# Performance work log

Measured on AMD Instinct MI355X. Metric: run time of the kernel, lower is better.

## Reference

```python
import jax, jax.numpy as jnp
import numpy as np
from jax import lax
from functools import lru_cache

WS = 8       # window size
SS = 4       # shift size
NH = 8       # attention heads
D_STATE = 64
D_CONV = 4
CHUNK = 256  # SSD chunk length


def _ln(x, w, b, eps=1e-5):
    mu = x.mean(-1, keepdims=True)
    xc = x - mu
    var = (xc * xc).mean(-1, keepdims=True)
    return xc * lax.rsqrt(var + eps) * w + b


@lru_cache(maxsize=None)
def _rel_index(ws):
    coords = np.stack(np.meshgrid(np.arange(ws), np.arange(ws), indexing='ij')).reshape(2, -1)
    rel = (coords[:, :, None] - coords[:, None, :]).transpose(1, 2, 0)
    rel[:, :, 0] += ws - 1
    rel[:, :, 1] += ws - 1
    rel[:, :, 0] *= 2 * ws - 1
    return jnp.asarray(rel.sum(-1))  # (N, N)


@lru_cache(maxsize=None)
def _shift_mask(H, W, ws, ss):
    img = np.zeros((H, W))
    cnt = 0
    for hs in (slice(0, -ws), slice(-ws, -ss), slice(-ss, None)):
        for wsl in (slice(0, -ws), slice(-ws, -ss), slice(-ss, None)):
            img[hs, wsl] = cnt
            cnt += 1
    mw = img.reshape(H // ws, ws, W // ws, ws).transpose(0, 2, 1, 3).reshape(-1, ws * ws)
    diff = mw[:, None, :] - mw[:, :, None]
    return jnp.asarray(np.where(diff != 0, -100.0, 0.0).astype(np.float32))  # (nW,N,N)


def _segsum(a):
    # a: (...,Q) -> (...,Q,Q) with S[i,j] = sum_{k=j+1..i} a_k for i>=j else -inf
    T = a.shape[-1]
    cs = jnp.cumsum(a, -1)
    d = cs[..., :, None] - cs[..., None, :]
    return jnp.where(jnp.tril(jnp.ones((T, T), bool)), d, -jnp.inf)


def _ssd(xd, a, Bc, Cc):
    # Chunked SSD scan (Mamba2). xd=(B,L,H,P) pre-multiplied by dt; a=dt*A (B,L,H);
    # Bc,Cc=(B,L,N) with ngroups=1 (shared across heads).
    B_, L, H_, P = xd.shape
    Q = CHUNK
    c = L // Q
    N = Bc.shape[-1]
    xd = xd.reshape(B_, c, Q, H_, P)
    a = a.reshape(B_, c, Q, H_).transpose(0, 3, 1, 2)  # (B,H,c,Q)
    Bc = Bc.reshape(B_, c, Q, N)
    Cc = Cc.reshape(B_, c, Q, N)
    A_cs = jnp.cumsum(a, -1)
    Lm = jnp.exp(_segsum(a))  # (B,H,c,Q,Q) causal decay mask
    Yd = jnp.einsum('bcln,bcsn,bhcls,bcshp->bclhp', Cc, Bc, Lm, xd)
    dec_st = jnp.exp(A_cs[..., -1:] - A_cs)
    states = jnp.einsum('bcsn,bhcs,bcshp->bchpn', Bc, dec_st, xd)  # (B,c,H,P,N)
    chunk_dec = jnp.exp(A_cs[..., -1])  # (B,H,c)

    def step(h, inp):
        dec, st = inp
        return h * dec[..., None, None] + st, h

    h0 = jnp.zeros((B_, H_, P, N), xd.dtype)
    _, st_in = lax.scan(step, h0, (chunk_dec.transpose(2, 0, 1), states.transpose(1, 0, 2, 3, 4)))
    st_in = st_in.transpose(1, 0, 2, 3, 4)  # (B,c,H,P,N) state entering each chunk
    Yo = jnp.einsum('bcln,bchpn,bhcl->bclhp', Cc, st_in, jnp.exp(A_cs))
    return (Yd + Yo).reshape(B_, L, H_, P)


def _mamba2(x, win, conv_w, conv_b, dt_bias, a_log, d_skip, norm_w, wout):
    Bb, L, _ = x.shape
    conv_dim = conv_w.shape[0]
    d_inner = conv_dim - 2 * D_STATE
    nh = a_log.shape[0]
    hd = d_inner // nh
    zxbcdt = x @ win
    z = zxbcdt[..., :d_inner]
    xBC = zxbcdt[..., d_inner:d_inner + conv_dim]
    dt = zxbcdt[..., -nh:]
    # causal depthwise conv (kernel D_CONV) + SiLU
    xp = jnp.pad(xBC, ((0, 0), (D_CONV - 1, 0), (0, 0)))
    xc = conv_b + sum(xp[:, k:k + L, :] * conv_w[:, k] for k in range(D_CONV))
    xc = jax.nn.silu(xc)
    xs = xc[..., :d_inner].reshape(Bb, L, nh, hd)
    Bm = xc[..., d_inner:d_inner + D_STATE]
    Cm = xc[..., d_inner + D_STATE:]
    dt = jax.nn.softplus(dt + dt_bias)  # (B,L,nh)
    a = dt * (-jnp.exp(a_log))
    y = _ssd(xs * dt[..., None], a, Bm, Cm)
    y = y + d_skip[None, None, :, None] * xs
    y = y.reshape(Bb, L, d_inner)
    u = y * jax.nn.silu(z)  # gated RMSNorm
    u = u * lax.rsqrt((u * u).mean(-1, keepdims=True) + 1e-5) * norm_w
    return u @ wout


def reference(x, ln1_w, ln1_b, ns_w, ns_b, m_win, m_conv_w, m_conv_b, m_dt_bias,
              m_a_log, m_d, m_norm_w, m_wout, tm_w1, tm_b1, tm_w2, tm_b2, nt_w, nt_b,
              qkv_w, qkv_b, rpb, gate_w, gate_b, proj_w, proj_b,
              cg_w1a, cg_b1a, cg_w2a, cg_b2a, cg_w1m, cg_b1m, cg_w2m, cg_b2m, cg_wf, cg_bf,
              ln2_w, ln2_b, mlp_w1, mlp_b1, mlp_w2, mlp_b2, H, W):
    twoB, L, C = x.shape
    B = twoB // 2
    shortcut = x
    xn = _ln(x, ln1_w, ln1_b)
    # ---- Branch A: factorized SSM (spatial Mamba2 + symmetric temporal MLP fusion) ----
    xns = _ln(xn, ns_w, ns_b)
    sp = _mamba2(xns, m_win, m_conv_w, m_conv_b, m_dt_bias, m_a_log, m_d, m_norm_w, m_wout) + xn
    f0, f1 = sp[:B], sp[B:]

    def tmix(a, b):
        h = jax.nn.silu(jnp.concatenate([a, b], -1) @ tm_w1 + tm_b1)
        return h @ tm_w2 + tm_b2

    f0 = _ln(f0 + tmix(f0, f1), nt_w, nt_b)
    f1 = _ln(f1 + tmix(f1, f0), nt_w, nt_b)
    xm = jnp.concatenate([f0, f1], 0)
    # ---- Branch B: shifted-window gated attention ----
    N = WS * WS
    x2 = jnp.roll(xn.reshape(twoB, H, W, C), (-SS, -SS), (1, 2))
    xw = x2.reshape(twoB, H // WS, WS, W // WS, WS, C).transpose(0, 1, 3, 2, 4, 5).reshape(-1, N, C)
    qkv = (xw @ qkv_w + qkv_b).reshape(-1, N, 3, NH, C // NH).transpose(2, 0, 3, 1, 4)
    q, k, v = qkv[0], qkv[1], qkv[2]  # (nWB, NH, N, hd)
    attn = (q * (C // NH) ** -0.5) @ k.transpose(0, 1, 3, 2)
    attn = attn + rpb[_rel_index(WS)].transpose(2, 0, 1)[None]
    mask = _shift_mask(H, W, WS, SS)
    nW = mask.shape[0]
    attn = (attn.reshape(twoB, nW, NH, N, N) + mask[None, :, None]).reshape(-1, NH, N, N)
    attn = jax.nn.softmax(attn, -1)
    out = (attn @ v).transpose(0, 2, 1, 3).reshape(-1, N, C)
    out = out * jax.nn.sigmoid(xw @ gate_w + gate_b)  # per-token gate
    out = out @ proj_w + proj_b
    out = out.reshape(twoB, H // WS, W // WS, WS, WS, C).transpose(0, 1, 3, 2, 4, 5).reshape(twoB, H, W, C)
    xa = jnp.roll(out, (SS, SS), (1, 2)).reshape(twoB, L, C)
    # ---- Cross-gating fusion (1x1-conv bottleneck gates == per-position MLPs) ----
    gm = jax.nn.sigmoid(jax.nn.relu(xa @ cg_w1a + cg_b1a) @ cg_w2a + cg_b2a)
    ga = jax.nn.sigmoid(jax.nn.relu(xm @ cg_w1m + cg_b1m) @ cg_w2m + cg_b2m)
    fused = jnp.concatenate([xm * gm, xa * ga], -1) @ cg_wf + cg_bf
    xo = shortcut + fused
    # ---- MLP ----
    h = jax.nn.gelu(_ln(xo, ln2_w, ln2_b) @ mlp_w1 + mlp_b1, approximate=False)
    return xo + h @ mlp_w2 + mlp_b2


def setup_inputs():
    key = jax.random.key(0)
    ks = iter(jax.random.split(key, 64))

    def nrm(shape, s=0.02):
        return jax.random.normal(next(ks), shape, jnp.float32) * s

    C, d_inner, nh_m = 256, 512, 8
    twoB, H, W = 8, 64, 64
    L = H * W
    conv_dim = d_inner + 2 * D_STATE
    inp = dict(
        x=jax.random.normal(next(ks), (twoB, L, C), jnp.float32),
        ln1_w=jnp.ones(C), ln1_b=jnp.zeros(C),
        ns_w=jnp.ones(C), ns_b=jnp.zeros(C),
        m_win=nrm((C, 2 * d_inner + 2 * D_STATE + nh_m)),
        m_conv_w=nrm((conv_dim, D_CONV), 0.1), m_conv_b=jnp.zeros(conv_dim),
        m_dt_bias=nrm((nh_m,), 0.1),
        m_a_log=jnp.log(jnp.arange(1, nh_m + 1, dtype=jnp.float32)),
        m_d=jnp.ones(nh_m), m_norm_w=jnp.ones(d_inner), m_wout=nrm((d_inner, C)),
        tm_w1=nrm((2 * C, C)), tm_b1=jnp.zeros(C), tm_w2=nrm((C, C)), tm_b2=jnp.zeros(C),
        nt_w=jnp.ones(C), nt_b=jnp.zeros(C),
        qkv_w=nrm((C, 3 * C)), qkv_b=jnp.zeros(3 * C),
        rpb=nrm(((2 * WS - 1) ** 2, NH)),
        gate_w=nrm((C, C)), gate_b=jnp.zeros(C),
        proj_w=nrm((C, C)), proj_b=jnp.zeros(C),
        cg_w1a=nrm((C, C // 4)), cg_b1a=jnp.zeros(C // 4), cg_w2a=nrm((C // 4, C)), cg_b2a=jnp.zeros(C),
        cg_w1m=nrm((C, C // 4)), cg_b1m=jnp.zeros(C // 4), cg_w2m=nrm((C // 4, C)), cg_b2m=jnp.zeros(C),
        cg_wf=nrm((2 * C, C)), cg_bf=jnp.zeros(C),
        ln2_w=jnp.ones(C), ln2_b=jnp.zeros(C),
        mlp_w1=nrm((C, 4 * C)), mlp_b1=jnp.zeros(4 * C),
        mlp_w2=nrm((4 * C, C)), mlp_b2=jnp.zeros(C),
        H=H, W=W,
    )
    return inp
```

## Files before the change

kernel.cpp:

```cpp
#include <hip/hip_runtime.h>
#include <math.h>


#define DEVI static __device__ __forceinline__
typedef unsigned short u16;
typedef unsigned int   u32;
typedef __attribute__((ext_vector_type(8))) short s16x8;
typedef __attribute__((ext_vector_type(4))) float f32x4;

DEVI float sigm_(float x){ return 1.f/(1.f+__expf(-x)); }
DEVI float silu_(float x){ return x/(1.f+__expf(-x)); }
DEVI float wsum_(float v){
#pragma unroll
  for (int o=32;o>0;o>>=1) v += __shfl_xor(v,o,64);
  return v;
}

DEVI float b2f(u16 u){ union{u32 i; float f;} v; v.i = ((u32)u)<<16; return v.f; }
DEVI u16 f2b(float f){ union{float f; u32 i;} v; v.f=f; u32 r = v.i + 0x7fffu + ((v.i>>16)&1u); return (u16)(r>>16); }
DEVI float4 ld4(const float* p){ return *(const float4*)p; }
DEVI float4 ld4(const u16* p){
  uint2 r = *(const uint2*)p;
  return make_float4(b2f((u16)(r.x&0xffff)), b2f((u16)(r.x>>16)),
                     b2f((u16)(r.y&0xffff)), b2f((u16)(r.y>>16)));
}
DEVI void st4(u16* p, float a, float b, float c, float d){
  uint2 r; r.x = (u32)f2b(a) | ((u32)f2b(b)<<16); r.y = (u32)f2b(c) | ((u32)f2b(d)<<16);
  *(uint2*)p = r;
}
DEVI void ld8(const u16* p, float* f){
  uint4 r = *(const uint4*)p;
  f[0]=b2f((u16)(r.x&0xffff)); f[1]=b2f((u16)(r.x>>16));
  f[2]=b2f((u16)(r.y&0xffff)); f[3]=b2f((u16)(r.y>>16));
  f[4]=b2f((u16)(r.z&0xffff)); f[5]=b2f((u16)(r.z>>16));
  f[6]=b2f((u16)(r.w&0xffff)); f[7]=b2f((u16)(r.w>>16));
}
DEVI void st8(u16* p, const float* f){
  uint4 r;
  r.x=(u32)f2b(f[0])|((u32)f2b(f[1])<<16); r.y=(u32)f2b(f[2])|((u32)f2b(f[3])<<16);
  r.z=(u32)f2b(f[4])|((u32)f2b(f[5])<<16); r.w=(u32)f2b(f[6])|((u32)f2b(f[7])<<16);
  *(uint4*)p = r;
}
DEVI float tof(float v){ return v; }
DEVI float tof(u16 v){ return b2f(v); }
DEVI void sto(float* p, float v){ *p = v; }
DEVI void sto(u16* p, float v){ *p = f2b(v); }

DEVI int vswz(int row, int ch){ return ch ^ ((row&7) ^ ((row>>3)&7)); }

DEVI void gl16(const u16* g, u16* l){
  __builtin_amdgcn_global_load_lds(
      (const __attribute__((address_space(1))) u32*)g,
      (__attribute__((address_space(3))) u32*)l, 16, 0, 0);
}

DEVI int winmap_tok(int r){
  int win = r>>6, tk = r&63;
  int b = win>>6, wid = win&63;
  int h2 = ((wid>>3)<<3) + (tk>>3);
  int w2 = ((wid&7)<<3) + (tk&7);
  int hh = (h2+4)&63, wwp = (w2+4)&63;
  return b*4096 + hh*64 + wwp;
}

__global__ __launch_bounds__(256) void ln2x_k(
    const float* __restrict__ x, const float* __restrict__ w1, const float* __restrict__ b1,
    const float* __restrict__ w2, const float* __restrict__ b2,
    u16* __restrict__ xn, u16* __restrict__ xns)
{
  int tok = blockIdx.x*4 + (threadIdx.x>>6);
  int lane = threadIdx.x & 63;
  size_t base = (size_t)tok*256 + lane*4;
  float4 v = *(const float4*)(x + base);
  float mu = wsum_(v.x+v.y+v.z+v.w) * (1.f/256.f);
  float ax=v.x-mu, ay=v.y-mu, az=v.z-mu, aw=v.w-mu;
  float var = wsum_(ax*ax+ay*ay+az*az+aw*aw) * (1.f/256.f);
  float r = rsqrtf(var+1e-5f);
  float4 wv = *(const float4*)(w1+lane*4);
  float4 bv = *(const float4*)(b1+lane*4);
  float ox=ax*r*wv.x+bv.x, oy=ay*r*wv.y+bv.y, oz=az*r*wv.z+bv.z, ow=aw*r*wv.w+bv.w;
  st4(xn + base, ox, oy, oz, ow);
  float mu2 = wsum_(ox+oy+oz+ow)*(1.f/256.f);
  float bx=ox-mu2, by=oy-mu2, bz=oz-mu2, bw=ow-mu2;
  float var2 = wsum_(bx*bx+by*by+bz*bz+bw*bw)*(1.f/256.f);
  float r2 = rsqrtf(var2+1e-5f);
  float4 w2v = *(const float4*)(w2+lane*4);
  float4 b2v = *(const float4*)(b2+lane*4);
  st4(xns + base, bx*r2*w2v.x+b2v.x, by*r2*w2v.y+b2v.y, bz*r2*w2v.z+b2v.z, bw*r2*w2v.w+b2v.w);
}

template<typename IT>
__global__ __launch_bounds__(256) void ln_k(
    const IT* __restrict__ in, const float* __restrict__ w, const float* __restrict__ b,
    u16* __restrict__ outp)
{
  int tok = blockIdx.x*4 + (threadIdx.x>>6);
  int lane = threadIdx.x & 63;
  size_t base = (size_t)tok*256 + lane*4;
  float4 v = ld4(in + base);
  float mu = wsum_(v.x+v.y+v.z+v.w) * (1.f/256.f);
  float ax=v.x-mu, ay=v.y-mu, az=v.z-mu, aw=v.w-mu;
  float var = wsum_(ax*ax+ay*ay+az*az+aw*aw) * (1.f/256.f);
  float r = rsqrtf(var+1e-5f);
  float4 wv = *(const float4*)(w+lane*4);
  float4 bv = *(const float4*)(b+lane*4);
  st4(outp + base, ax*r*wv.x+bv.x, ay*r*wv.y+bv.y, az*r*wv.z+bv.z, aw*r*wv.w+bv.w);
}

struct WtD { const float* W; u16* Wt; int ldw, K, kb, nt; };
struct WtTab { WtD d[15]; };

__global__ __launch_bounds__(256) void wtall_k(WtTab tab)
{
  int loc = blockIdx.x;
  int r = 0;
#pragma unroll
  for (int i=0;i<15;i++){
    int cnt = tab.d[i].kb * tab.d[i].nt;
    if (loc >= cnt && r == i){ loc -= cnt; r = i+1; }
  }
  const float* W = tab.d[r].W;
  u16* Wt = tab.d[r].Wt;
  int ldw = tab.d[r].ldw, K = tab.d[r].K, kb = tab.d[r].kb;
  int k0 = (loc % kb)*32, n0 = (loc / kb)*32;
  __shared__ float tl[32][33];
  int t = threadIdx.x; int ty=t>>5, tx=t&31;
#pragma unroll
  for (int i=0;i<4;i++){
    int k = ty + i*8;
    tl[k][tx] = W[(size_t)(k0+k)*ldw + n0+tx];
  }
  __syncthreads();
#pragma unroll
  for (int i=0;i<4;i++){
    int n = ty + i*8;
    Wt[(size_t)(n0+n)*K + k0 + tx] = f2b(tl[tx][n]);
  }
}

enum { EPI_NONE=0, EPI_SILU=1, EPI_GELU=2, EPI_SIGMUL=3, EPI_ADD=4, EPI_RELU=5, EPI_SIGMOID=6 };

template<int BM, int BN, int EPI, bool WIN, bool WINST, typename OT, typename CT>
__global__ __launch_bounds__(256) void mgemm_k(
    const u16* __restrict__ A1, const u16* __restrict__ A2, int K1, int K2,
    const u16* __restrict__ Wt, const float* __restrict__ bias,
    const OT* other, CT* outp, int N, int r0)
{
  constexpr int MW = BM/32;
  constexpr int NWF = BN/32;
  constexpr int LA = BM/32;
  constexpr int LB = BN/32;
  __shared__ u16 As[BM][64];
  __shared__ u16 Bs[BN][64];
  int m0 = blockIdx.y*BM, n0 = blockIdx.x*BN;
  int t = threadIdx.x;
  int lane = t&63, w = t>>6;
  int wr = w>>1, wc = w&1;
  int K = K1 + K2;
  f32x4 acc[MW][NWF];
#pragma unroll
  for (int mi=0;mi<MW;mi++)
#pragma unroll
    for (int ni=0;ni<NWF;ni++) acc[mi][ni] = (f32x4){0.f,0.f,0.f,0.f};
  int srow = lane>>3;
  int cs   = ((lane&7) ^ srow)*8;
  size_t aoff1[LA], aoff2[LA];
#pragma unroll
  for (int i=0;i<LA;i++){
    int gr = m0 + i*32 + w*8 + srow;
    if (WIN) aoff1[i] = (size_t)winmap_tok(r0+gr)*K1;
    else { aoff1[i] = (size_t)gr*K1; aoff2[i] = (size_t)gr*K2; }
  }
  size_t boff[LB];
#pragma unroll
  for (int i=0;i<LB;i++)
    boff[i] = (size_t)(n0 + i*32 + w*8 + srow)*K;
  for (int k0=0; k0<K; k0+=64){
#pragma unroll
    for (int i=0;i<LA;i++){
      const u16* ap = (WIN || k0 < K1) ? A1 + aoff1[i] + k0 + cs
                                       : A2 + aoff2[i] + (k0-K1) + cs;
      gl16(ap, &As[i*32 + w*8][0]);
    }
#pragma unroll
    for (int i=0;i<LB;i++){
      gl16(Wt + boff[i] + k0 + cs, &Bs[i*32 + w*8][0]);
    }
    __syncthreads();
    int lg = lane>>4, li = lane&15;
#pragma unroll
    for (int kk=0;kk<2;kk++){
      s16x8 afr[MW], bfr[NWF];
#pragma unroll
      for (int mi=0;mi<MW;mi++){
        int lr = wr*(BM/2)+mi*16+li;
        afr[mi] = *(const s16x8*)&As[lr][(((kk<<2)+lg) ^ (lr&7))<<3];
      }
#pragma unroll
      for (int ni=0;ni<NWF;ni++){
        int lr = wc*(BN/2)+ni*16+li;
        bfr[ni] = *(const s16x8*)&Bs[lr][(((kk<<2)+lg) ^ (lr&7))<<3];
      }
#pragma unroll
      for (int mi=0;mi<MW;mi++)
#pragma unroll
        for (int ni=0;ni<NWF;ni++)
          acc[mi][ni] = __builtin_amdgcn_mfma_f32_16x16x32_bf16(afr[mi], bfr[ni], acc[mi][ni], 0,0,0);
    }
    __syncthreads();
  }
  int lg = lane>>4, li = lane&15;
#pragma unroll
  for (int mi=0;mi<MW;mi++){
#pragma unroll
    for (int ni=0;ni<NWF;ni++){
      int gn = n0 + wc*(BN/2) + ni*16 + li;
      float bv = bias ? bias[gn] : 0.f;
#pragma unroll
      for (int r=0;r<4;r++){
        int gm = m0 + wr*(BM/2) + mi*16 + lg*4 + r;
        float v = acc[mi][ni][r] + bv;
        size_t orow = WINST ? (size_t)winmap_tok(r0+gm) : (size_t)gm;
        size_t off = orow*N + gn;
        if (EPI==EPI_SILU)        v = silu_(v);
        else if (EPI==EPI_GELU)   v = 0.5f*v*(1.f+erff(v*0.70710678118654752f));
        else if (EPI==EPI_SIGMUL) v = tof(other[off])*sigm_(v);
        else if (EPI==EPI_ADD)    v = v + tof(other[off]);
        else if (EPI==EPI_RELU)   v = fmaxf(v,0.f);
        else if (EPI==EPI_SIGMOID)v = sigm_(v);
        sto(outp + off, v);
      }
    }
  }
}

template<int EPI, typename OT, typename CT>
__global__ __launch_bounds__(256) void gemm_k(
    const u16* __restrict__ A1, const u16* __restrict__ A2, int K1, int K2,
    const float* __restrict__ W, int ldw, const float* __restrict__ bias,
    const OT* other, CT* outp, int M, int N)
{
  __shared__ float as[16][68];
  __shared__ float bs[16][64];
  int m0 = blockIdx.y*64, n0 = blockIdx.x*64;
  int t = threadIdx.x;
  int ty = t>>4, tx = t&15;
  float acc[4][4] = {{0.f}};
  int K = K1 + K2;
  int arow = t>>2, ac4 = (t&3)<<2;
  int bkr = t>>4, bnc = (t&15)<<2;
  for (int k0=0; k0<K; k0+=16){
    int gk = k0 + ac4;
    float4 av;
    if (gk < K1) av = ld4(A1 + (size_t)(m0+arow)*K1 + gk);
    else         av = ld4(A2 + (size_t)(m0+arow)*K2 + (gk-K1));
    as[ac4+0][arow]=av.x; as[ac4+1][arow]=av.y; as[ac4+2][arow]=av.z; as[ac4+3][arow]=av.w;
    int gn = n0 + bnc;
    const float* wp = W + (size_t)(k0+bkr)*ldw;
    if (gn+3 < N) {
      *(float4*)&bs[bkr][bnc] = *(const float4*)(wp + gn);
    } else {
#pragma unroll
      for (int j=0;j<4;j++) bs[bkr][bnc+j] = (gn+j<N) ? wp[gn+j] : 0.f;
    }
    __syncthreads();
#pragma unroll
    for (int kk=0; kk<16; kk++){
      float4 a4 = *(const float4*)&as[kk][ty*4];
      float4 b4 = *(const float4*)&bs[kk][tx*4];
      acc[0][0]+=a4.x*b4.x; acc[0][1]+=a4.x*b4.y; acc[0][2]+=a4.x*b4.z; acc[0][3]+=a4.x*b4.w;
      acc[1][0]+=a4.y*b4.x; acc[1][1]+=a4.y*b4.y; acc[1][2]+=a4.y*b4.z; acc[1][3]+=a4.y*b4.w;
      acc[2][0]+=a4.z*b4.x; acc[2][1]+=a4.z*b4.y; acc[2][2]+=a4.z*b4.z; acc[2][3]+=a4.z*b4.w;
      acc[3][0]+=a4.w*b4.x; acc[3][1]+=a4.w*b4.y; acc[3][2]+=a4.w*b4.z; acc[3][3]+=a4.w*b4.w;
    }
    __syncthreads();
  }
#pragma unroll
  for (int i=0;i<4;i++){
    int gm = m0 + ty*4 + i;
#pragma unroll
    for (int j=0;j<4;j++){
      int gn = n0 + tx*4 + j;
      if (gn >= N) continue;
      float v = acc[i][j] + (bias ? bias[gn] : 0.f);
      size_t off = (size_t)gm*N + gn;
      if (EPI==EPI_SILU)        v = silu_(v);
      else if (EPI==EPI_GELU)   v = 0.5f*v*(1.f+erff(v*0.70710678118654752f));
      else if (EPI==EPI_SIGMUL) v = tof(other[off])*sigm_(v);
      else if (EPI==EPI_ADD)    v = v + tof(other[off]);
      else if (EPI==EPI_RELU)   v = fmaxf(v,0.f);
      else if (EPI==EPI_SIGMOID)v = sigm_(v);
      sto(outp + off, v);
    }
  }
}

__global__ __launch_bounds__(256) void xbcconv_k(
    const u16* __restrict__ A1, const u16* __restrict__ Wt,
    const float* __restrict__ cw, const float* __restrict__ cb,
    u16* __restrict__ XC)
{
  __shared__ u16 As[64][40];
  __shared__ u16 Ab[16][40];
  __shared__ u16 Bs[128][40];
  __shared__ float Cls[67][132];
  int m0 = blockIdx.y*64, n0 = blockIdx.x*128;
  bool first = ((m0 & 4095) == 0);
  int t = threadIdx.x;
  int lane = t&63, w = t>>6;
  int wr = w>>1, wc = w&1;
  int lg = lane>>4, li = lane&15;
  f32x4 acc[2][4], acc3[2];
#pragma unroll
  for (int mi=0;mi<2;mi++)
#pragma unroll
    for (int ni=0;ni<4;ni++) acc[mi][ni] = (f32x4){0.f,0.f,0.f,0.f};
  acc3[0]=(f32x4){0,0,0,0}; acc3[1]=(f32x4){0,0,0,0};
  for (int i=t; i<320; i+=256) ((u32*)&Ab[0][0])[i] = 0u;
  int lrow = t>>2, lc8 = (t&3)*8;
  for (int k0=0; k0<256; k0+=32){
    *(uint4*)&As[lrow][lc8] = *(const uint4*)(A1 + (size_t)(m0+lrow)*256 + k0 + lc8);
    if (t < 12 && !first){
      int r3 = t>>2, seg = t&3;
      *(uint4*)&Ab[r3][seg*8] = *(const uint4*)(A1 + (size_t)(m0-3+r3)*256 + k0 + seg*8);
    }
#pragma unroll
    for (int i=0;i<2;i++){
      int row = lrow + i*64;
      *(uint4*)&Bs[row][lc8] = *(const uint4*)(Wt + (size_t)(n0+row)*256 + k0 + lc8);
    }
    __syncthreads();
    s16x8 afr[2], bfr[4];
#pragma unroll
    for (int mi=0;mi<2;mi++)
      afr[mi] = *(const s16x8*)&As[wr*32+mi*16+li][lg*8];
#pragma unroll
    for (int ni=0;ni<4;ni++)
      bfr[ni] = *(const s16x8*)&Bs[wc*64+ni*16+li][lg*8];
#pragma unroll
    for (int mi=0;mi<2;mi++)
#pragma unroll
      for (int ni=0;ni<4;ni++)
        acc[mi][ni] = __builtin_amdgcn_mfma_f32_16x16x32_bf16(afr[mi], bfr[ni], acc[mi][ni], 0,0,0);
    {
      s16x8 abf = *(const s16x8*)&Ab[li][lg*8];
#pragma unroll
      for (int ni2=0;ni2<2;ni2++){
        s16x8 bb = *(const s16x8*)&Bs[w*32+ni2*16+li][lg*8];
        acc3[ni2] = __builtin_amdgcn_mfma_f32_16x16x32_bf16(abf, bb, acc3[ni2], 0,0,0);
      }
    }
    __syncthreads();
  }
#pragma unroll
  for (int mi=0;mi<2;mi++)
#pragma unroll
    for (int ni=0;ni<4;ni++){
      int col = wc*64 + ni*16 + li;
#pragma unroll
      for (int r=0;r<4;r++){
        int rl = wr*32 + mi*16 + lg*4 + r;
        Cls[3+rl][col] = acc[mi][ni][r];
      }
    }
  if (lg == 0){
#pragma unroll
    for (int ni2=0;ni2<2;ni2++){
      int col = w*32 + ni2*16 + li;
#pragma unroll
      for (int r=0;r<3;r++)
        Cls[r][col] = acc3[ni2][r];
    }
  }
  __syncthreads();
  int col = t & 127, half = t >> 7;
  int ch = n0 + col;
  float w0 = cw[ch*4+0], w1 = cw[ch*4+1], w2 = cw[ch*4+2], w3 = cw[ch*4+3];
  float bias = cb[ch];
  int r0 = half*32;
  float c0 = Cls[r0+0][col], c1 = Cls[r0+1][col], c2 = Cls[r0+2][col];
#pragma unroll
  for (int rr=0; rr<32; rr++){
    float c3 = Cls[r0+rr+3][col];
    float v = bias + w0*c0 + w1*c1 + w2*c2 + w3*c3;
    XC[(size_t)(m0 + r0 + rr)*640 + ch] = f2b(silu_(v));
    c0=c1; c1=c2; c2=c3;
  }
}

__global__ __launch_bounds__(256) void dtk_k(
    const float* __restrict__ DTRAW, const float* __restrict__ dtb, const float* __restrict__ alog,
    float* __restrict__ DT_, float* __restrict__ AA_)
{
  int gid = blockIdx.x*256 + threadIdx.x;
  int h = gid & 7;
  float xv = DTRAW[gid] + dtb[h];
  float sp = (xv > 20.f) ? xv : log1pf(__expf(xv));
  DT_[gid] = sp;
  AA_[gid] = -sp * __expf(alog[h]);
}

__global__ __launch_bounds__(256) void acs_k(const float* __restrict__ AA_, float* __restrict__ ACS_)
{
  int wid = (blockIdx.x<<2) + (threadIdx.x>>6);
  int lane = threadIdx.x & 63;
  int c  = wid & 15;
  int bh = wid >> 4;
  int b  = bh >> 3, h = bh & 7;
  size_t tok0 = (size_t)b*4096 + c*256 + lane*4;
  float v0 = AA_[(tok0+0)*8 + h];
  float v1 = AA_[(tok0+1)*8 + h];
  float v2 = AA_[(tok0+2)*8 + h];
  float v3 = AA_[(tok0+3)*8 + h];
  v1 += v0; v2 += v1; v3 += v2;
  float tot = v3, s = tot;
#pragma unroll
  for (int o=1;o<64;o<<=1){
    float u = __shfl_up(s, o, 64);
    if (lane >= o) s += u;
  }
  float excl = s - tot;
  float* dst = ACS_ + (size_t)bh*4096 + c*256 + lane*4;
  dst[0]=excl+v0; dst[1]=excl+v1; dst[2]=excl+v2; dst[3]=excl+v3;
}

__global__ __launch_bounds__(256) void states_k(
    const u16* __restrict__ XC, const float* __restrict__ DTc, const float* __restrict__ ACSc,
    float* __restrict__ ST)
{
  int b = blockIdx.x;
  int j = b & 7, s = b >> 3;
  int h = s & 7, gq = s >> 3;
  int g = j + gq*8;
  int c = g & 15, bl = g >> 4;
  __shared__ u16 Xt[64*64];
  __shared__ u16 Bt[64*64];
  int t = threadIdx.x;
  int lane = t&63, w = t>>6;
  int wr = w>>1, wc = w&1;
  int lg = lane>>4, li = lane&15;
  const float* acs = ACSc + ((size_t)(bl*8+h))*4096 + c*256;
  float aL = acs[255];
  size_t tok0 = (size_t)bl*4096 + c*256;
  f32x4 acc[2][2];
#pragma unroll
  for (int mi=0;mi<2;mi++)
#pragma unroll
    for (int ni=0;ni<2;ni++) acc[mi][ni] = (f32x4){0.f,0.f,0.f,0.f};
  int sr = t>>2, cg = t&3;
  int srch = sr>>3, srlo = sr&7;
  for (int s0=0; s0<256; s0+=64){
    __syncthreads();
    size_t grow = tok0 + s0 + sr;
    float dtv = DTc[grow*8 + h];
    float wdec = __expf(aL - acs[s0+sr]);
    const u16* xrow = XC + grow*640 + h*64 + cg*16;
    const u16* brow = XC + grow*640 + 512 + cg*16;
    uint4 xa = *(const uint4*)xrow, xb = *(const uint4*)(xrow+8);
    uint4 ba = *(const uint4*)brow, bb = *(const uint4*)(brow+8);
    const u16* xu = (const u16*)&xa;
    const u16* bu = (const u16*)&ba;
#pragma unroll
    for (int jj=0;jj<8;jj++){
      int row = cg*16+jj;
      int off = row*64 + (vswz(row,srch)<<3) + srlo;
      Xt[off] = f2b(b2f(xu[jj])*dtv);
      Bt[off] = f2b(b2f(bu[jj])*wdec);
    }
    const u16* xu2 = (const u16*)&xb;
    const u16* bu2 = (const u16*)&bb;
#pragma unroll
    for (int jj=0;jj<8;jj++){
      int row = cg*16+8+jj;
      int off = row*64 + (vswz(row,srch)<<3) + srlo;
      Xt[off] = f2b(b2f(xu2[jj])*dtv);
      Bt[off] = f2b(b2f(bu2[jj])*wdec);
    }
    __syncthreads();
    s16x8 afr[2][2], bfr[2][2];
#pragma unroll
    for (int kk=0;kk<2;kk++){
#pragma unroll
      for (int mi=0;mi<2;mi++){
        int row = wr*32+mi*16+li;
        afr[mi][kk] = *(const s16x8*)&Xt[row*64 + (vswz(row, kk*4+lg)<<3)];
      }
#pragma unroll
      for (int ni=0;ni<2;ni++){
        int row = wc*32+ni*16+li;
        bfr[ni][kk] = *(const s16x8*)&Bt[row*64 + (vswz(row, kk*4+lg)<<3)];
      }
    }
#pragma unroll
    for (int kk=0;kk<2;kk++)
#pragma unroll
      for (int mi=0;mi<2;mi++)
#pragma unroll
        for (int ni=0;ni<2;ni++)
          acc[mi][ni] = __builtin_amdgcn_mfma_f32_16x16x32_bf16(afr[mi][kk], bfr[ni][kk], acc[mi][ni], 0,0,0);
  }
  float* dst = ST + ((size_t)(g*8 + h))*4096;
#pragma unroll
  for (int mi=0;mi<2;mi++)
#pragma unroll
    for (int ni=0;ni<2;ni++){
      int gn = wc*32 + ni*16 + li;
#pragma unroll
      for (int r=0;r<4;r++){
        int gp = wr*32 + mi*16 + lg*4 + r;
        dst[gp*64 + gn] = acc[mi][ni][r];
      }
    }
}

__global__ __launch_bounds__(256) void scan_k(
    const float* __restrict__ ST, const float* __restrict__ ACSc, u16* __restrict__ STIN)
{
  int bid = blockIdx.x;
  int eq = bid & 3, h = (bid>>2)&7, bl = bid>>5;
  int t = threadIdx.x;
  float hr[4] = {0.f,0.f,0.f,0.f};
  for (int c=0;c<16;c++){
    float dec = __expf(ACSc[((size_t)(bl*8+h))*4096 + c*256 + 255]);
    size_t base = ((size_t)((bl*16+c)*8+h))*4096 + (size_t)eq*1024;
#pragma unroll
    for (int e=0;e<4;e++){
      size_t idx = base + e*256 + t;
      float st = ST[idx];
      STIN[idx] = f2b(hr[e]);
      hr[e] = hr[e]*dec + st;
    }
  }
}

__global__ __launch_bounds__(256) void ydy_k(
    const u16* __restrict__ XC, const float* __restrict__ DTc,
    const float* __restrict__ ACSc, const u16* __restrict__ STIN,
    const float* __restrict__ dskip, u16* __restrict__ Y)
{
  int b = blockIdx.x;
  int j = b & 7, s = b >> 3;
  int lt = s & 3, h = (s>>2) & 7, gq = s >> 5;
  int g = j + gq*8;
  int c = g & 15, bl = g >> 4;
  int l0 = lt*64;
  __shared__ u16 Ct[64][72];
  __shared__ u16 Sb[64][72];
  __shared__ u16 Sl[64][72];
  __shared__ u16 Vt[64*64];
  int t = threadIdx.x;
  int lane = t&63, w = t>>6;
  int wr = w>>1, wc = w&1;
  int lg = lane>>4, li = lane&15;
  const float* acs = ACSc + ((size_t)(bl*8+h))*4096 + c*256;
  size_t tok0 = (size_t)bl*4096 + c*256;
  int sr = t>>2;
#pragma unroll
  for (int it=0; it<2; it++){
    int seg = (t&3) + it*4;
    *(uint4*)&Ct[sr][seg*8] = *(const uint4*)(XC + (tok0+l0+sr)*640 + 576 + seg*8);
  }
  float acsl[2][4];
#pragma unroll
  for (int mi=0;mi<2;mi++)
#pragma unroll
    for (int r=0;r<4;r++)
      acsl[mi][r] = acs[l0 + wr*32 + mi*16 + lg*4 + r];
  f32x4 accP[2][2], accO[2][2];
#pragma unroll
  for (int mi=0;mi<2;mi++)
#pragma unroll
    for (int ni=0;ni<2;ni++){ accP[mi][ni]=(f32x4){0,0,0,0}; accO[mi][ni]=(f32x4){0,0,0,0}; }
  __syncthreads();
  const u16* stin = STIN + ((size_t)(g*8+h))*4096;
#pragma unroll
  for (int kk=0;kk<2;kk++){
    s16x8 bfr[2];
#pragma unroll
    for (int ni=0;ni<2;ni++){
      int p = wc*32 + ni*16 + li;
      bfr[ni] = *(const s16x8*)(stin + p*64 + kk*32 + lg*8);
    }
#pragma unroll
    for (int mi=0;mi<2;mi++){
      s16x8 afr = *(const s16x8*)&Ct[wr*32+mi*16+li][kk*32+lg*8];
#pragma unroll
      for (int ni=0;ni<2;ni++)
        accO[mi][ni] = __builtin_amdgcn_mfma_f32_16x16x32_bf16(afr, bfr[ni], accO[mi][ni], 0,0,0);
    }
  }
  int cg = t&3;
  int srch = sr>>3, srlo = sr&7;
  for (int sb=0; sb<=lt; sb++){
    int s0 = sb*64;
    __syncthreads();
#pragma unroll
    for (int it=0; it<2; it++){
      int seg = (t&3) + it*4;
      *(uint4*)&Sb[sr][seg*8] = *(const uint4*)(XC + (tok0+s0+sr)*640 + 512 + seg*8);
    }
    {
      size_t grow = tok0 + s0 + sr;
      const u16* xrow = XC + grow*640 + h*64 + cg*16;
      uint4 xa = *(const uint4*)xrow, xb = *(const uint4*)(xrow+8);
      const u16* xu = (const u16*)&xa;
#pragma unroll
      for (int jj=0;jj<8;jj++){
        int row = cg*16+jj;
        Vt[row*64 + (vswz(row,srch)<<3) + srlo] = xu[jj];
      }
      const u16* xu2 = (const u16*)&xb;
#pragma unroll
      for (int jj=0;jj<8;jj++){
        int row = cg*16+8+jj;
        Vt[row*64 + (vswz(row,srch)<<3) + srlo] = xu2[jj];
      }
    }
    __syncthreads();
    f32x4 sacc[2][2];
#pragma unroll
    for (int mi=0;mi<2;mi++)
#pragma unroll
      for (int ni=0;ni<2;ni++) sacc[mi][ni]=(f32x4){0,0,0,0};
#pragma unroll
    for (int kk=0;kk<2;kk++){
      s16x8 bfr[2];
#pragma unroll
      for (int ni=0;ni<2;ni++)
        bfr[ni] = *(const s16x8*)&Sb[wc*32+ni*16+li][kk*32+lg*8];
#pragma unroll
      for (int mi=0;mi<2;mi++){
        s16x8 afr = *(const s16x8*)&Ct[wr*32+mi*16+li][kk*32+lg*8];
#pragma unroll
        for (int ni=0;ni<2;ni++)
          sacc[mi][ni] = __builtin_amdgcn_mfma_f32_16x16x32_bf16(afr, bfr[ni], sacc[mi][ni], 0,0,0);
      }
    }
#pragma unroll
    for (int ni=0;ni<2;ni++){
      int cs2 = wc*32 + ni*16 + li;
      int gsj = s0 + cs2;
      float acss = acs[gsj];
      float dts = DTc[(tok0+gsj)*8 + h];
#pragma unroll
      for (int mi=0;mi<2;mi++){
#pragma unroll
        for (int r=0;r<4;r++){
          int lrow = wr*32 + mi*16 + lg*4 + r;
          int gl = l0 + lrow;
          float wgt = (gsj <= gl) ? __expf(acsl[mi][r] - acss)*dts : 0.f;
          Sl[lrow][cs2] = f2b(sacc[mi][ni][r] * wgt);
        }
      }
    }
    __syncthreads();
#pragma unroll
    for (int kk=0;kk<2;kk++){
      s16x8 bfr[2];
#pragma unroll
      for (int ni=0;ni<2;ni++){
        int p = wc*32+ni*16+li;
        bfr[ni] = *(const s16x8*)&Vt[p*64 + (vswz(p, kk*4+lg)<<3)];
      }
#pragma unroll
      for (int mi=0;mi<2;mi++){
        s16x8 afr = *(const s16x8*)&Sl[wr*32+mi*16+li][kk*32+lg*8];
#pragma unroll
        for (int ni=0;ni<2;ni++)
          accP[mi][ni] = __builtin_amdgcn_mfma_f32_16x16x32_bf16(afr, bfr[ni], accP[mi][ni], 0,0,0);
      }
    }
  }
  __syncthreads();
  float dsk = dskip[h];
#pragma unroll
  for (int mi=0;mi<2;mi++){
#pragma unroll
    for (int ni=0;ni<2;ni++){
      int p = wc*32 + ni*16 + li;
#pragma unroll
      for (int r=0;r<4;r++){
        int lrow = wr*32 + mi*16 + lg*4 + r;
        float el = __expf(acsl[mi][r]);
        float xsv = b2f(Vt[p*64 + (vswz(p, lrow>>3)<<3) + (lrow&7)]);
        Sb[lrow][p] = f2b(accP[mi][ni][r] + el*accO[mi][ni][r] + dsk*xsv);
      }
    }
  }
  __syncthreads();
#pragma unroll
  for (int it=0; it<2; it++){
    int seg = (t&3) + it*4;
    *(uint4*)(Y + (tok0+l0+sr)*512 + h*64 + seg*8) = *(const uint4*)&Sb[sr][seg*8];
  }
}

__global__ __launch_bounds__(256) void urms_k(
    u16* Y, const u16* __restrict__ Z, const float* __restrict__ nw)
{
  int tok = blockIdx.x*4 + (threadIdx.x>>6);
  int lane = threadIdx.x & 63;
  size_t base = (size_t)tok*512 + lane*8;
  float y[8], z[8], u[8];
  ld8(Y+base, y); ld8(Z+base, z);
  float ss=0.f;
#pragma unroll
  for (int e=0;e<8;e++){ u[e] = y[e]*silu_(z[e]); ss += u[e]*u[e]; }
  ss = wsum_(ss);
  float r = rsqrtf(ss*(1.f/512.f) + 1e-5f);
  float4 w0 = *(const float4*)(nw + lane*8);
  float4 w1 = *(const float4*)(nw + lane*8 + 4);
  float o[8];
  o[0]=u[0]*r*w0.x; o[1]=u[1]*r*w0.y; o[2]=u[2]*r*w0.z; o[3]=u[3]*r*w0.w;
  o[4]=u[4]*r*w1.x; o[5]=u[5]*r*w1.y; o[6]=u[6]*r*w1.z; o[7]=u[7]*r*w1.w;
  st8(Y+base, o);
}

__global__ __launch_bounds__(256) void attn_k(
    const u16* __restrict__ QKV, const float* __restrict__ rpb, u16* __restrict__ OW)
{
  int win = blockIdx.x;
  int wid = win & 63;
  int head = blockIdx.y;
  __shared__ u16 Qs[64][40];
  __shared__ u16 Ks[64][40];
  __shared__ u16 Vt[32][72];
  __shared__ u16 Pl[64][72];
  __shared__ float rl[225];
  __shared__ int rid[64];
  int t = threadIdx.x;
  int lane = t&63, w = t>>6;
  int lg = lane>>4, li = lane&15;
  const float scale = 0.17677669529663687f;
  {
    int row = t>>2, seg = t&3;
    const u16* base = QKV + ((size_t)win*64 + row)*768 + head*32 + seg*8;
    uint4 q = *(const uint4*)base;
    const u16* qe = (const u16*)&q;
    u16 qs8[8];
#pragma unroll
    for (int jq=0;jq<8;jq++) qs8[jq] = f2b(b2f(qe[jq])*scale);
    *(uint4*)&Qs[row][seg*8] = *(const uint4*)qs8;
    *(uint4*)&Ks[row][seg*8] = *(const uint4*)(base + 256);
    uint4 v = *(const uint4*)(base + 512);
    const u16* ve = (const u16*)&v;
#pragma unroll
    for (int jq=0;jq<8;jq++) Vt[seg*8+jq][row] = ve[jq];
  }
  if (t < 225) rl[t] = rpb[t*8 + head];
  if (t < 64){
    int h2 = ((wid>>3)<<3) + (t>>3);
    int w2 = ((wid&7)<<3) + (t&7);
    int rh = (h2<56)?0:((h2<60)?1:2);
    int rw = (w2<56)?0:((w2<60)?1:2);
    rid[t] = rh*3 + rw;
  }
  __syncthreads();
  f32x4 sc[4];
  {
    s16x8 qf = *(const s16x8*)&Qs[w*16+li][lg*8];
#pragma unroll
    for (int ni=0;ni<4;ni++){
      s16x8 kf = *(const s16x8*)&Ks[ni*16+li][lg*8];
      sc[ni] = __builtin_amdgcn_mfma_f32_16x16x32_bf16(qf, kf, (f32x4){0,0,0,0}, 0,0,0);
    }
  }
  float inv[4];
#pragma unroll
  for (int r=0;r<4;r++){
    int i = w*16 + lg*4 + r;
    int ridi = rid[i];
    float vv[4];
    float m = -1e30f;
#pragma unroll
    for (int ni=0;ni<4;ni++){
      int jj = ni*16 + li;
      float sv = sc[ni][r] + rl[((i>>3)-(jj>>3)+7)*15 + ((i&7)-(jj&7)+7)];
      if (ridi != rid[jj]) sv -= 100.f;
      vv[ni] = sv;
      m = fmaxf(m, sv);
    }
#pragma unroll
    for (int o=1;o<16;o<<=1) m = fmaxf(m, __shfl_xor(m, o, 64));
    float sum = 0.f;
#pragma unroll
    for (int ni=0;ni<4;ni++){ vv[ni] = __expf(vv[ni]-m); sum += vv[ni]; }
#pragma unroll
    for (int o=1;o<16;o<<=1) sum += __shfl_xor(sum, o, 64);
    inv[r] = 1.f/sum;
#pragma unroll
    for (int ni=0;ni<4;ni++) Pl[i][ni*16+li] = f2b(vv[ni]);
  }
  __syncthreads();
  f32x4 oacc[2];
  oacc[0]=(f32x4){0,0,0,0}; oacc[1]=(f32x4){0,0,0,0};
#pragma unroll
  for (int kk=0;kk<2;kk++){
    s16x8 pf = *(const s16x8*)&Pl[w*16+li][kk*32+lg*8];
#pragma unroll
    for (int ni=0;ni<2;ni++){
      s16x8 vf = *(const s16x8*)&Vt[ni*16+li][kk*32+lg*8];
      oacc[ni] = __builtin_amdgcn_mfma_f32_16x16x32_bf16(pf, vf, oacc[ni], 0,0,0);
    }
  }
#pragma unroll
  for (int ni=0;ni<2;ni++)
#pragma unroll
    for (int r=0;r<4;r++)
      Pl[w*16+lg*4+r][ni*16+li] = f2b(oacc[ni][r]*inv[r]);
  __syncthreads();
  {
    int row = t>>2, seg = t&3;
    *(uint4*)(OW + ((size_t)win*64 + row)*256 + head*32 + seg*8) = *(const uint4*)&Pl[row][seg*8];
  }
}

extern "C" void kernel_launch(void* const* d_in, const int* in_sizes, int n_in,
                              void* d_out, int out_size, void* d_ws, size_t ws_size,
                              hipStream_t stream)
{
  (void)in_sizes; (void)n_in; (void)out_size;
  const size_t OFF_XN   = 0;
  const size_t OFF_XNS  = 16777216;
  const size_t OFF_SP   = 33554432;
  const size_t OFF_DTRAW= 50331648;
  const size_t OFF_DT   = 51380224;
  const size_t OFF_AA   = 52428800;
  const size_t OFF_ACS  = 53477376;
  const size_t OFF_WTS  = 54525952;
  const size_t ARO      = 58195968;
  int NB = 0;
  if      (ws_size >= ARO + 8ull*14680064) NB = 8;
  else if (ws_size >= ARO + 4ull*14680064) NB = 4;
  else if (ws_size >= ARO + 2ull*14680064) NB = 2;
  else if (ws_size >= ARO + 1ull*14680064) NB = 1;
  else return;
  int NC = 8 / NB;
  int RJ = (NB==8)?32768 : (NB==4)?16384 : (NB==2)?8192 : 4096;

  const float* x       = (const float*)d_in[0];
  const float* ln1_w   = (const float*)d_in[1];
  const float* ln1_b   = (const float*)d_in[2];
  const float* ns_w    = (const float*)d_in[3];
  const float* ns_b    = (const float*)d_in[4];
  const float* m_win   = (const float*)d_in[5];
  const float* m_conv_w= (const float*)d_in[6];
  const float* m_conv_b= (const float*)d_in[7];
  const float* m_dt_b  = (const float*)d_in[8];
  const float* m_a_log = (const float*)d_in[9];
  const float* m_d     = (const float*)d_in[10];
  const float* m_norm_w= (const float*)d_in[11];
  const float* m_wout  = (const float*)d_in[12];
  const float* tm_w1   = (const float*)d_in[13];
  const float* tm_b1   = (const float*)d_in[14];
  const float* tm_w2   = (const float*)d_in[15];
  const float* tm_b2   = (const float*)d_in[16];
  const float* nt_w    = (const float*)d_in[17];
  const float* nt_b    = (const float*)d_in[18];
  const float* qkv_w   = (const float*)d_in[19];
  const float* qkv_b   = (const float*)d_in[20];
  const float* rpb     = (const float*)d_in[21];
  const float* gate_w  = (const float*)d_in[22];
  const float* gate_b  = (const float*)d_in[23];
  const float* proj_w  = (const float*)d_in[24];
  const float* proj_b  = (const float*)d_in[25];
  const float* cg_w1a  = (const float*)d_in[26];
  const float* cg_b1a  = (const float*)d_in[27];
  const float* cg_w2a  = (const float*)d_in[28];
  const float* cg_b2a  = (const float*)d_in[29];
  const float* cg_w1m  = (const float*)d_in[30];
  const float* cg_b1m  = (const float*)d_in[31];
  const float* cg_w2m  = (const float*)d_in[32];
  const float* cg_b2m  = (const float*)d_in[33];
  const float* cg_wf   = (const float*)d_in[34];
  const float* cg_bf   = (const float*)d_in[35];
  const float* ln2_w   = (const float*)d_in[36];
  const float* ln2_b   = (const float*)d_in[37];
  const float* mlp_w1  = (const float*)d_in[38];
  const float* mlp_b1  = (const float*)d_in[39];
  const float* mlp_w2  = (const float*)d_in[40];
  const float* mlp_b2  = (const float*)d_in[41];
  float* dout = (float*)d_out;
  char* ws = (char*)d_ws;

  u16*  XN   = (u16*)(ws + OFF_XN);
  u16*  XNS  = (u16*)(ws + OFF_XNS);
  u16*  SP   = (u16*)(ws + OFF_SP);
  float* DTRAW = (float*)(ws + OFF_DTRAW);
  float* DT  = (float*)(ws + OFF_DT);
  float* AA  = (float*)(ws + OFF_AA);
  float* ACS = (float*)(ws + OFF_ACS);
  u16*  WTS  = (u16*)(ws + OFF_WTS);
  u16* WT_XBC = WTS + 0;
  u16* WT_Z   = WTS + 163840;
  u16* WT_WOUT= WTS + 294912;
  u16* WT_TM1 = WTS + 425984;
  u16* WT_TM2 = WTS + 491520;
  u16* WT_QKV = WTS + 557056;
  u16* WT_GATE= WTS + 753664;
  u16* WT_PROJ= WTS + 819200;
  u16* WT_W2A = WTS + 884736;
  u16* WT_W2M = WTS + 901120;
  u16* WT_WF  = WTS + 917504;
  u16* WT_MLP1= WTS + 1048576;
  u16* WT_MLP2= WTS + 1310720;
  u16* WT_W1A = WTS + 1572864;
  u16* WT_W1M = WTS + 1589248;
  char* AR = ws + ARO;
  u16*  XCc   = (u16*)AR;
  u16*  Zc    = (u16*)(AR + (size_t)NB*5242880);
  u16*  STINc = (u16*)(AR + (size_t)NB*9437184);
  float* STc  = (float*)(AR + (size_t)NB*10485760);
  u16*  Yc    = (u16*)(AR + (size_t)NB*10485760);
  u16*  QKVc  = (u16*)AR;
  u16*  OWc   = (u16*)(AR + (size_t)NB*6291456);
  u16*  TBUF  = (u16*)AR;
  u16*  XM    = XNS;
  u16*  XA    = XN;
  u16*  CGHA  = (u16*)AR;
  u16*  CGHM  = (u16*)(AR + 4194304);
  u16*  LNc   = (u16*)AR;
  u16*  MHc   = (u16*)(AR + (size_t)RJ*512);

  const size_t TB = 4096*256;
  const size_t H2 = 16384*256;

  WtTab tab;
  tab.d[0]  = { m_win+512, WT_XBC, 1160, 256, 8, 20 };
  tab.d[1]  = { m_win,     WT_Z,   1160, 256, 8, 16 };
  tab.d[2]  = { m_wout,    WT_WOUT, 256, 512, 16, 8 };
  tab.d[3]  = { tm_w1,     WT_TM1,  256, 512, 16, 8 };
  tab.d[4]  = { tm_w2,     WT_TM2,  256, 256, 8, 8 };
  tab.d[5]  = { qkv_w,     WT_QKV,  768, 256, 8, 24 };
  tab.d[6]  = { gate_w,    WT_GATE, 256, 256, 8, 8 };
  tab.d[7]  = { proj_w,    WT_PROJ, 256, 256, 8, 8 };
  tab.d[8]  = { cg_w2a,    WT_W2A,  256, 64, 2, 8 };
  tab.d[9]  = { cg_w2m,    WT_W2M,  256, 64, 2, 8 };
  tab.d[10] = { cg_wf,     WT_WF,   256, 512, 16, 8 };
  tab.d[11] = { mlp_w1,    WT_MLP1,1024, 256, 8, 32 };
  tab.d[12] = { mlp_w2,    WT_MLP2, 256,1024, 32, 8 };
  tab.d[13] = { cg_w1a,    WT_W1A,   64, 256, 8, 2 };
  tab.d[14] = { cg_w1m,    WT_W1M,   64, 256, 8, 2 };
  int ntiles = 0;
  for (int i=0;i<15;i++) ntiles += tab.d[i].kb * tab.d[i].nt;
  wtall_k<<<ntiles,256,0,stream>>>(tab);

  ln2x_k<<<8192,256,0,stream>>>(x, ln1_w, ln1_b, ns_w, ns_b, XN, XNS);
  gemm_k<EPI_NONE,float,float><<<dim3(1,512),256,0,stream>>>(XNS,nullptr,256,0, m_win+1152,1160, nullptr, nullptr, DTRAW, 32768,8);
  dtk_k<<<1024,256,0,stream>>>(DTRAW, m_dt_b, m_a_log, DT, AA);
  acs_k<<<256,256,0,stream>>>(AA, ACS);

  for (int cc=0; cc<NC; cc++){
    int cb0 = cc*NB;
    const u16* XNSc = XNS + (size_t)cb0*TB;
    const float* DTcp = DT + (size_t)cb0*32768;
    const float* ACScp = ACS + (size_t)cb0*32768;
    xbcconv_k<<<dim3(5,NB*64),256,0,stream>>>(XNSc, WT_XBC, m_conv_w, m_conv_b, XCc);
    states_k<<<NB*128,256,0,stream>>>(XCc, DTcp, ACScp, STc);
    scan_k<<<NB*32,256,0,stream>>>(STc, ACScp, STINc);
    ydy_k<<<NB*512,256,0,stream>>>(XCc, DTcp, ACScp, STINc, m_d, Yc);
    mgemm_k<128,128,EPI_NONE,false,false,float,u16><<<dim3(4,NB*32),256,0,stream>>>(XNSc,nullptr,256,0, WT_Z, nullptr, nullptr, Zc, 512, 0);
    urms_k<<<NB*1024,256,0,stream>>>(Yc, Zc, m_norm_w);
    mgemm_k<128,128,EPI_ADD,false,false,u16,u16><<<dim3(2,NB*32),256,0,stream>>>(Yc,nullptr,512,0, WT_WOUT, nullptr, XN + (size_t)cb0*TB, SP + (size_t)cb0*TB, 256, 0);
  }

  mgemm_k<128,128,EPI_SILU,false,false,float,u16><<<dim3(2,128),256,0,stream>>>(SP, SP+H2, 256,256, WT_TM1, tm_b1, nullptr, TBUF, 256, 0);
  mgemm_k<128,128,EPI_ADD,false,false,u16,u16><<<dim3(2,128),256,0,stream>>>(TBUF,nullptr,256,0, WT_TM2, tm_b2, SP, XM, 256, 0);
  ln_k<u16><<<4096,256,0,stream>>>(XM, nt_w, nt_b, XM);
  mgemm_k<128,128,EPI_SILU,false,false,float,u16><<<dim3(2,128),256,0,stream>>>(SP+H2, XM, 256,256, WT_TM1, tm_b1, nullptr, TBUF, 256, 0);
  mgemm_k<128,128,EPI_ADD,false,false,u16,u16><<<dim3(2,128),256,0,stream>>>(TBUF,nullptr,256,0, WT_TM2, tm_b2, SP+H2, XM+H2, 256, 0);
  ln_k<u16><<<4096,256,0,stream>>>(XM+H2, nt_w, nt_b, XM+H2);

  for (int cc=0; cc<NC; cc++){
    int r0 = cc*NB*4096;
    mgemm_k<128,128,EPI_NONE,true,false,float,u16><<<dim3(6,NB*32),256,0,stream>>>(XN,nullptr,256,0, WT_QKV, qkv_b, nullptr, QKVc, 768, r0);
    attn_k<<<dim3(NB*64,8),256,0,stream>>>(QKVc, rpb, OWc);
    mgemm_k<128,128,EPI_SIGMUL,true,false,u16,u16><<<dim3(2,NB*32),256,0,stream>>>(XN,nullptr,256,0, WT_GATE, gate_b, OWc, OWc, 256, r0);
    mgemm_k<128,128,EPI_NONE,false,true,float,u16><<<dim3(2,NB*32),256,0,stream>>>(OWc,nullptr,256,0, WT_PROJ, proj_b, nullptr, XA, 256, r0);
  }

  mgemm_k<128,64,EPI_RELU,false,false,float,u16><<<dim3(1,256),256,0,stream>>>(XA,nullptr,256,0, WT_W1A, cg_b1a, nullptr, CGHA, 64, 0);
  mgemm_k<128,64,EPI_RELU,false,false,float,u16><<<dim3(1,256),256,0,stream>>>(XM,nullptr,256,0, WT_W1M, cg_b1m, nullptr, CGHM, 64, 0);
  mgemm_k<128,128,EPI_SIGMUL,false,false,u16,u16><<<dim3(2,256),256,0,stream>>>(CGHA,nullptr,64,0, WT_W2A, cg_b2a, XM, XM, 256, 0);
  mgemm_k<128,128,EPI_SIGMUL,false,false,u16,u16><<<dim3(2,256),256,0,stream>>>(CGHM,nullptr,64,0, WT_W2M, cg_b2m, XA, XA, 256, 0);
  mgemm_k<128,128,EPI_ADD,false,false,float,float><<<dim3(2,256),256,0,stream>>>(XM, XA, 256,256, WT_WF, cg_bf, x, dout, 256, 0);

  for (int q=0; q<32768/RJ; q++){
    float* XOq = dout + (size_t)q*RJ*256;
    ln_k<float><<<RJ/4,256,0,stream>>>(XOq, ln2_w, ln2_b, LNc);
    mgemm_k<128,128,EPI_GELU,false,false,float,u16><<<dim3(8,RJ/128),256,0,stream>>>(LNc,nullptr,256,0, WT_MLP1, mlp_b1, nullptr, MHc, 1024, 0);
    mgemm_k<128,128,EPI_ADD,false,false,float,float><<<dim3(2,RJ/128),256,0,stream>>>(MHc,nullptr,1024,0, WT_MLP2, mlp_b2, XOq, XOq, 256, 0);
  }
}
```

Baseline: 623.1 us.

## Emit transposed X from conv kernel so SSD kernels load it with vector copies

The conv epilogue now also writes a chunk-transposed copy of the x channels (head-dim major, token minor) into the Z buffer region, which is free until the Z GEMM runs. states_k and ydy_k then fill their shared-memory X tiles with 16-byte vector loads and stores instead of scattered per-element transposed writes. In states_k the dt factor is moved from X onto the B-side decay scale, so X no longer needs a per-element multiply. The cost is an extra global write in the conv kernel and a small change in bf16 rounding, since dt is now folded into B.

```diff
diff --git a/kernel.cpp b/kernel.cpp
--- a/kernel.cpp
+++ b/kernel.cpp
@@ -298,7 +298,7 @@
 __global__ __launch_bounds__(256) void xbcconv_k(
     const u16* __restrict__ A1, const u16* __restrict__ Wt,
     const float* __restrict__ cw, const float* __restrict__ cb,
-    u16* __restrict__ XC)
+    u16* __restrict__ XC, u16* __restrict__ XT)
 {
   __shared__ u16 As[64][40];
   __shared__ u16 Ab[16][40];
@@ -379,12 +379,21 @@
   float bias = cb[ch];
   int r0 = half*32;
   float c0 = Cls[r0+0][col], c1 = Cls[r0+1][col], c2 = Cls[r0+2][col];
+  u16 xtbuf[32];
 #pragma unroll
   for (int rr=0; rr<32; rr++){
     float c3 = Cls[r0+rr+3][col];
     float v = bias + w0*c0 + w1*c1 + w2*c2 + w3*c3;
-    XC[(size_t)(m0 + r0 + rr)*640 + ch] = f2b(silu_(v));
+    u16 bv16 = f2b(silu_(v));
+    XC[(size_t)(m0 + r0 + rr)*640 + ch] = bv16;
+    xtbuf[rr] = bv16;
     c0=c1; c1=c2; c2=c3;
+  }
+  if (ch < 512){
+    int g = m0 >> 8;
+    u16* dst = XT + ((size_t)(g*512 + ch))*256 + (m0&255) + r0;
+#pragma unroll
+    for (int q=0;q<4;q++) *(uint4*)(dst + q*8) = *(const uint4*)&xtbuf[q*8];
   }
 }
 
@@ -425,7 +434,8 @@
 }
 
 __global__ __launch_bounds__(256) void states_k(
-    const u16* __restrict__ XC, const float* __restrict__ DTc, const float* __restrict__ ACSc,
+    const u16* __restrict__ XC, const u16* __restrict__ XT,
+    const float* __restrict__ DTc, const float* __restrict__ ACSc,
     float* __restrict__ ST)
 {
   int b = blockIdx.x;
@@ -449,32 +459,34 @@
     for (int ni=0;ni<2;ni++) acc[mi][ni] = (f32x4){0.f,0.f,0.f,0.f};
   int sr = t>>2, cg = t&3;
   int srch = sr>>3, srlo = sr&7;
+  const u16* xtb = XT + ((size_t)(g*512) + h*64)*256;
   for (int s0=0; s0<256; s0+=64){
     __syncthreads();
-    size_t grow = tok0 + s0 + sr;
-    float dtv = DTc[grow*8 + h];
-    float wdec = __expf(aL - acs[s0+sr]);
-    const u16* xrow = XC + grow*640 + h*64 + cg*16;
-    const u16* brow = XC + grow*640 + 512 + cg*16;
-    uint4 xa = *(const uint4*)xrow, xb = *(const uint4*)(xrow+8);
-    uint4 ba = *(const uint4*)brow, bb = *(const uint4*)(brow+8);
-    const u16* xu = (const u16*)&xa;
-    const u16* bu = (const u16*)&ba;
-#pragma unroll
-    for (int jj=0;jj<8;jj++){
-      int row = cg*16+jj;
-      int off = row*64 + (vswz(row,srch)<<3) + srlo;
-      Xt[off] = f2b(b2f(xu[jj])*dtv);
-      Bt[off] = f2b(b2f(bu[jj])*wdec);
-    }
-    const u16* xu2 = (const u16*)&xb;
-    const u16* bu2 = (const u16*)&bb;
-#pragma unroll
-    for (int jj=0;jj<8;jj++){
-      int row = cg*16+8+jj;
-      int off = row*64 + (vswz(row,srch)<<3) + srlo;
-      Xt[off] = f2b(b2f(xu2[jj])*dtv);
-      Bt[off] = f2b(b2f(bu2[jj])*wdec);
+    {
+      int prow = t>>2, c2 = t&3;
+      const u16* src = xtb + (size_t)prow*256 + s0;
+      uint4 a0 = *(const uint4*)(src + c2*8);
+      uint4 a1 = *(const uint4*)(src + (c2+4)*8);
+      *(uint4*)&Xt[prow*64 + (vswz(prow,c2)<<3)]   = a0;
+      *(uint4*)&Xt[prow*64 + (vswz(prow,c2+4)<<3)] = a1;
+    }
+    {
+      size_t grow = tok0 + s0 + sr;
+      float scl = __expf(aL - acs[s0+sr]) * DTc[grow*8 + h];
+      const u16* brow_p = XC + grow*640 + 512 + cg*16;
+      uint4 ba = *(const uint4*)brow_p, bb2 = *(const uint4*)(brow_p+8);
+      const u16* bu = (const u16*)&ba;
+#pragma unroll
+      for (int jj=0;jj<8;jj++){
+        int row = cg*16+jj;
+        Bt[row*64 + (vswz(row,srch)<<3) + srlo] = f2b(b2f(bu[jj])*scl);
+      }
+      const u16* bu2 = (const u16*)&bb2;
+#pragma unroll
+      for (int jj=0;jj<8;jj++){
+        int row = cg*16+8+jj;
+        Bt[row*64 + (vswz(row,srch)<<3) + srlo] = f2b(b2f(bu2[jj])*scl);
+      }
     }
     __syncthreads();
     s16x8 afr[2][2], bfr[2][2];
@@ -534,7 +546,8 @@
 }
 
 __global__ __launch_bounds__(256) void ydy_k(
-    const u16* __restrict__ XC, const float* __restrict__ DTc,
+    const u16* __restrict__ XC, const u16* __restrict__ XT,
+    const float* __restrict__ DTc,
     const float* __restrict__ ACSc, const u16* __restrict__ STIN,
     const float* __restrict__ dskip, u16* __restrict__ Y)
 {
@@ -589,8 +602,7 @@
         accO[mi][ni] = __builtin_amdgcn_mfma_f32_16x16x32_bf16(afr, bfr[ni], accO[mi][ni], 0,0,0);
     }
   }
-  int cg = t&3;
-  int srch = sr>>3, srlo = sr&7;
+  const u16* xtb = XT + ((size_t)(g*512) + h*64)*256;
   for (int sb=0; sb<=lt; sb++){
     int s0 = sb*64;
     __syncthreads();
@@ -600,21 +612,12 @@
       *(uint4*)&Sb[sr][seg*8] = *(const uint4*)(XC + (tok0+s0+sr)*640 + 512 + seg*8);
     }
     {
-      size_t grow = tok0 + s0 + sr;
-      const u16* xrow = XC + grow*640 + h*64 + cg*16;
-      uint4 xa = *(const uint4*)xrow, xb = *(const uint4*)(xrow+8);
-      const u16* xu = (const u16*)&xa;
-#pragma unroll
-      for (int jj=0;jj<8;jj++){
-        int row = cg*16+jj;
-        Vt[row*64 + (vswz(row,srch)<<3) + srlo] = xu[jj];
-      }
-      const u16* xu2 = (const u16*)&xb;
-#pragma unroll
-      for (int jj=0;jj<8;jj++){
-        int row = cg*16+8+jj;
-        Vt[row*64 + (vswz(row,srch)<<3) + srlo] = xu2[jj];
-      }
+      int prow = t>>2, c2 = t&3;
+      const u16* src = xtb + (size_t)prow*256 + s0;
+      uint4 a0 = *(const uint4*)(src + c2*8);
+      uint4 a1 = *(const uint4*)(src + (c2+4)*8);
+      *(uint4*)&Vt[prow*64 + (vswz(prow,c2)<<3)]   = a0;
+      *(uint4*)&Vt[prow*64 + (vswz(prow,c2+4)<<3)] = a1;
     }
     __syncthreads();
     f32x4 sacc[2][2];
@@ -909,6 +912,7 @@
   char* AR = ws + ARO;
   u16*  XCc   = (u16*)AR;
   u16*  Zc    = (u16*)(AR + (size_t)NB*5242880);
+  u16*  XTc   = Zc;
   u16*  STINc = (u16*)(AR + (size_t)NB*9437184);
   float* STc  = (float*)(AR + (size_t)NB*10485760);
   u16*  Yc    = (u16*)(AR + (size_t)NB*10485760);
@@ -955,10 +959,10 @@
     const u16* XNSc = XNS + (size_t)cb0*TB;
     const float* DTcp = DT + (size_t)cb0*32768;
     const float* ACScp = ACS + (size_t)cb0*32768;
-    xbcconv_k<<<dim3(5,NB*64),256,0,stream>>>(XNSc, WT_XBC, m_conv_w, m_conv_b, XCc);
-    states_k<<<NB*128,256,0,stream>>>(XCc, DTcp, ACScp, STc);
+    xbcconv_k<<<dim3(5,NB*64),256,0,stream>>>(XNSc, WT_XBC, m_conv_w, m_conv_b, XCc, XTc);
+    states_k<<<NB*128,256,0,stream>>>(XCc, XTc, DTcp, ACScp, STc);
     scan_k<<<NB*32,256,0,stream>>>(STc, ACScp, STINc);
-    ydy_k<<<NB*512,256,0,stream>>>(XCc, DTcp, ACScp, STINc, m_d, Yc);
+    ydy_k<<<NB*512,256,0,stream>>>(XCc, XTc, DTcp, ACScp, STINc, m_d, Yc);
     mgemm_k<128,128,EPI_NONE,false,false,float,u16><<<dim3(4,NB*32),256,0,stream>>>(XNSc,nullptr,256,0, WT_Z, nullptr, nullptr, Zc, 512, 0);
     urms_k<<<NB*1024,256,0,stream>>>(Yc, Zc, m_norm_w);
     mgemm_k<128,128,EPI_ADD,false,false,u16,u16><<<dim3(2,NB*32),256,0,stream>>>(Yc,nullptr,512,0, WT_WOUT, nullptr, XN + (size_t)cb0*TB, SP + (size_t)cb0*TB, 256, 0);
```

After: 622.1 us. About the same (-0.2%).
